# Optimization experiments

Measured on AMD Instinct MI355X. Metric: run time of the kernel, lower is better.

## Reference

```python
import jax, jax.numpy as jnp
import numpy as np

B, C, H, W = 1024, 3, 32, 32
NCLS = 10

def _conv(x, w, b, padding):
    y = jax.lax.conv_general_dilated(x, w, (1, 1), padding, dimension_numbers=('NCHW', 'OIHW', 'NCHW'))
    return y + b[None, :, None, None]

def _maxpool2(x):
    return jax.lax.reduce_window(x, -jnp.inf, jax.lax.max, (1, 1, 2, 2), (1, 1, 2, 2), 'VALID')

def _lenet(x, lw1, lb1, lw2, lb2, lfc1, lfb1, lfc2, lfb2, lfc3, lfb3):
    h = jax.nn.relu(_conv(x, lw1, lb1, 'VALID'))   # [B,6,28,28]
    h = _maxpool2(h)                               # [B,6,14,14]
    h = jax.nn.relu(_conv(h, lw2, lb2, 'VALID'))   # [B,16,10,10]
    h = _maxpool2(h)                               # [B,16,5,5]
    h = h.reshape(h.shape[0], -1)                  # [B,400]
    h = jax.nn.relu(h @ lfc1 + lfb1)
    h = jax.nn.relu(h @ lfc2 + lfb2)
    return h @ lfc3 + lfb3                         # [B,10]

def _resnet(x, rw0, rb0, rw1a, rb1a, rw1b, rb1b, rw2a, rb2a, rw2b, rb2b, rfc, rfb):
    h = jax.nn.relu(_conv(x, rw0, rb0, 'SAME'))    # [B,64,32,32]
    r = jax.nn.relu(_conv(h, rw1a, rb1a, 'SAME'))
    r = _conv(r, rw1b, rb1b, 'SAME')
    h = jax.nn.relu(h + r)
    r = jax.nn.relu(_conv(h, rw2a, rb2a, 'SAME'))
    r = _conv(r, rw2b, rb2b, 'SAME')
    h = jax.nn.relu(h + r)
    h = h.mean(axis=(2, 3))                        # [B,64]
    return h @ rfc + rfb                           # [B,10]

def setup_inputs():
    key = jax.random.key(0)
    ks = jax.random.split(key, 16)
    def w(k, shape, fan_in):
        return jax.random.normal(k, shape, jnp.float32) * np.float32(1.0 / np.sqrt(fan_in))
    return {
        'x': jax.random.normal(ks[0], (B, C, H, W), jnp.float32),
        'threshold': jnp.float32(0.3),
        'labels': jax.random.randint(ks[1], (B,), 0, NCLS),
        'lw1': w(ks[2], (6, 3, 5, 5), 75), 'lb1': jnp.zeros((6,), jnp.float32),
        'lw2': w(ks[3], (16, 6, 5, 5), 150), 'lb2': jnp.zeros((16,), jnp.float32),
        'lfc1': w(ks[4], (400, 120), 400), 'lfb1': jnp.zeros((120,), jnp.float32),
        'lfc2': w(ks[5], (120, 84), 120), 'lfb2': jnp.zeros((84,), jnp.float32),
        'lfc3': w(ks[6], (84, NCLS), 84), 'lfb3': jnp.zeros((NCLS,), jnp.float32),
        'rw0': w(ks[7], (64, 3, 3, 3), 27), 'rb0': jnp.zeros((64,), jnp.float32),
        'rw1a': w(ks[8], (64, 64, 3, 3), 576), 'rb1a': jnp.zeros((64,), jnp.float32),
        'rw1b': w(ks[9], (64, 64, 3, 3), 576), 'rb1b': jnp.zeros((64,), jnp.float32),
        'rw2a': w(ks[10], (64, 64, 3, 3), 576), 'rb2a': jnp.zeros((64,), jnp.float32),
        'rw2b': w(ks[11], (64, 64, 3, 3), 576), 'rb2b': jnp.zeros((64,), jnp.float32),
        'rfc': w(ks[12], (64, NCLS), 64), 'rfb': jnp.zeros((NCLS,), jnp.float32),
    }

def reference(x, threshold, labels, lw1, lb1, lw2, lb2, lfc1, lfb1, lfc2, lfb2, lfc3, lfb3, rw0, rb0, rw1a, rb1a, rw1b, rb1b, rw2a, rb2a, rw2b, rb2b, rfc, rfb):
    out = _lenet(x, lw1, lb1, lw2, lb2, lfc1, lfb1, lfc2, lfb2, lfc3, lfb3)
    pred = jnp.argmax(out, axis=1)
    # fused confusion-matrix update: single scatter-add replaces the 10x10 python loop
    conf_matrix = jnp.zeros((NCLS, NCLS), jnp.float32).at[labels, pred].add(1.0)
    probs = jax.nn.softmax(out, axis=1)
    top2, _ = jax.lax.top_k(probs, 2)
    low_conf = (top2[:, 0] - top2[:, 1]) <= threshold    # [B] bool
    # batched fallback: one grouped resnet call + masked merge replaces the per-sample loop
    res_out = _resnet(x, rw0, rb0, rw1a, rb1a, rw1b, rb1b, rw2a, rb2a, rw2b, rb2b, rfc, rfb)
    out = jnp.where(low_conf[:, None], res_out, out)
    return out, conf_matrix
```

## Files before the change

### kernel.cpp

```cpp
#include <hip/hip_runtime.h>
#include <hip/hip_bf16.h>
#include <math.h>

#define BATCH 1024

typedef __attribute__((ext_vector_type(8))) short bf16x8;
typedef __attribute__((ext_vector_type(4))) float f32x4;

#define IMG_ELEMS 73984
#define IMG_B 147968
#define ROW_B 4352
#define CH_B 544
#define WT_OFF 43520
#define WT_HALF_B 36864
#define BOUNCE_OFF 25088
#define STAGE_A_U 1568

__global__ __launch_bounds__(256) void lenet_conv1(const float* __restrict__ x,
    const float* __restrict__ w, const float* __restrict__ bias, float* __restrict__ p1)
{
    __shared__ float img[3 * 1024];
    __shared__ float wl[450];
    __shared__ float bl[6];
    int b = blockIdx.x, t = threadIdx.x;
    for (int i = t; i < 3072; i += 256) img[i] = x[(size_t)b * 3072 + i];
    for (int i = t; i < 450; i += 256) wl[i] = w[i];
    if (t < 6) bl[t] = bias[t];
    __syncthreads();
    for (int idx = t; idx < 1176; idx += 256) {
        int o = idx / 196, r = idx - o * 196, py = r / 14, px = r - py * 14;
        int y0 = 2 * py, x0 = 2 * px;
        float s00, s01, s10, s11;
        s00 = s01 = s10 = s11 = bl[o];
        for (int c = 0; c < 3; c++) {
            float pv[6][6];
            #pragma unroll
            for (int i2 = 0; i2 < 6; i2++)
                #pragma unroll
                for (int j2 = 0; j2 < 6; j2++)
                    pv[i2][j2] = img[c * 1024 + (y0 + i2) * 32 + x0 + j2];
            const float* wc = &wl[o * 75 + c * 25];
            #pragma unroll
            for (int ky = 0; ky < 5; ky++)
                #pragma unroll
                for (int kx = 0; kx < 5; kx++) {
                    float wv = wc[ky * 5 + kx];
                    s00 += pv[ky][kx] * wv;
                    s01 += pv[ky][kx + 1] * wv;
                    s10 += pv[ky + 1][kx] * wv;
                    s11 += pv[ky + 1][kx + 1] * wv;
                }
        }
        float m = fmaxf(fmaxf(s00, s01), fmaxf(s10, s11));
        p1[(size_t)b * 1176 + idx] = fmaxf(m, 0.f);
    }
}

__global__ __launch_bounds__(256) void lenet_conv2(const float* __restrict__ p1,
    const float* __restrict__ w, const float* __restrict__ bias, float* __restrict__ p2)
{
    __shared__ float img[1176];
    __shared__ float wl[2400];
    __shared__ float bl[16];
    int b = blockIdx.x, t = threadIdx.x;
    for (int i = t; i < 1176; i += 256) img[i] = p1[(size_t)b * 1176 + i];
    for (int i = t; i < 2400; i += 256) wl[i] = w[i];
    if (t < 16) bl[t] = bias[t];
    __syncthreads();
    for (int idx = t; idx < 400; idx += 256) {
        int o = idx / 25, r = idx - o * 25, py = r / 5, px = r - py * 5;
        int y0 = 2 * py, x0 = 2 * px;
        float s00, s01, s10, s11;
        s00 = s01 = s10 = s11 = bl[o];
        for (int c = 0; c < 6; c++) {
            float pv[6][6];
            #pragma unroll
            for (int i2 = 0; i2 < 6; i2++)
                #pragma unroll
                for (int j2 = 0; j2 < 6; j2++)
                    pv[i2][j2] = img[c * 196 + (y0 + i2) * 14 + x0 + j2];
            const float* wc = &wl[o * 150 + c * 25];
            #pragma unroll
            for (int ky = 0; ky < 5; ky++)
                #pragma unroll
                for (int kx = 0; kx < 5; kx++) {
                    float wv = wc[ky * 5 + kx];
                    s00 += pv[ky][kx] * wv;
                    s01 += pv[ky][kx + 1] * wv;
                    s10 += pv[ky + 1][kx] * wv;
                    s11 += pv[ky + 1][kx + 1] * wv;
                }
        }
        float m = fmaxf(fmaxf(s00, s01), fmaxf(s10, s11));
        p2[(size_t)b * 400 + idx] = fmaxf(m, 0.f);
    }
}

__global__ __launch_bounds__(256) void lenet_fc(const float* __restrict__ p2,
    const float* __restrict__ w1, const float* __restrict__ b1,
    const float* __restrict__ w2, const float* __restrict__ b2,
    const float* __restrict__ w3, const float* __restrict__ b3,
    const int* __restrict__ labels, const float* __restrict__ thr,
    float* __restrict__ out, float* __restrict__ conf, int* __restrict__ flags)
{
    __shared__ float xin[400];
    __shared__ float h1[120];
    __shared__ float h2[84];
    __shared__ float ps[256];
    __shared__ float lg[10];
    int b = blockIdx.x, t = threadIdx.x;
    for (int i = t; i < 400; i += 256) xin[i] = p2[(size_t)b * 400 + i];
    __syncthreads();
    {
        int n = t & 127, half = t >> 7;
        float s = 0.f;
        if (n < 120) {
            int k0 = half * 200;
            for (int k = k0; k < k0 + 200; k++) s += xin[k] * w1[k * 120 + n];
        }
        ps[t] = s;
    }
    __syncthreads();
    if (t < 120) h1[t] = fmaxf(ps[t] + ps[t + 128] + b1[t], 0.f);
    __syncthreads();
    {
        int n = t & 127, half = t >> 7;
        float s = 0.f;
        if (n < 84) {
            int k0 = half * 60;
            for (int k = k0; k < k0 + 60; k++) s += h1[k] * w2[k * 84 + n];
        }
        ps[t] = s;
    }
    __syncthreads();
    if (t < 84) h2[t] = fmaxf(ps[t] + ps[t + 128] + b2[t], 0.f);
    __syncthreads();
    if (t < 10) {
        float s = b3[t];
        for (int k = 0; k < 84; k++) s += h2[k] * w3[k * 10 + t];
        lg[t] = s;
        out[(size_t)b * 10 + t] = s;
    }
    __syncthreads();
    if (t == 0) {
        int pred = 0;
        float m = lg[0];
        #pragma unroll
        for (int j = 1; j < 10; j++) if (lg[j] > m) { m = lg[j]; pred = j; }
        float se = 0.f, m2 = -1e30f;
        #pragma unroll
        for (int j = 0; j < 10; j++) {
            se += expf(lg[j] - m);
            if (j != pred) m2 = fmaxf(m2, lg[j]);
        }
        float gap = (1.f - expf(m2 - m)) / se;
        flags[b] = (gap <= thr[0]) ? 1 : 0;
        atomicAdd(&conf[labels[b] * 10 + pred], 1.f);
    }
}

__global__ __launch_bounds__(256) void prep_weights(
    const float* __restrict__ w0, const float* __restrict__ w1,
    const float* __restrict__ w2, const float* __restrict__ w3,
    __hip_bfloat16* __restrict__ dst)
{
    int tid = blockIdx.x * 256 + threadIdx.x;
    if (tid >= 4 * 36864) return;
    int c = tid / 36864, r = tid - c * 36864;
    int tap = r / 4096, r2 = r - tap * 4096;
    int co = r2 >> 6, ci = r2 & 63;
    const float* src = (c == 0) ? w0 : (c == 1) ? w1 : (c == 2) ? w2 : w3;
    float v = src[((size_t)co * 64 + ci) * 9 + tap];
    int nh = co >> 5, nt = (co >> 4) & 1, m = co & 15;
    int kb = ci >> 5, q = (ci >> 3) & 3, e = ci & 7;
    size_t elem = (size_t)(c * 2 + nh) * 18432
                + (size_t)((tap * 2 + kb) * 2 + nt) * 512 + q * 128 + m * 8 + e;
    dst[elem] = __float2bfloat16(v);
}

__global__ __launch_bounds__(256) void prep_w0t(const float* __restrict__ w,
                                                float* __restrict__ dst)
{
    int tid = blockIdx.x * 256 + threadIdx.x;
    if (tid >= 1728) return;
    int k = tid >> 6, co = tid & 63;
    dst[tid] = w[co * 27 + k];
}

__global__ __launch_bounds__(256) void zero_borders(__hip_bfloat16* __restrict__ buf, int cb)
{
    int tid = blockIdx.x * 256 + threadIdx.x;
    int total = cb * 132 * 8;
    if (tid >= total) return;
    int img = tid / 1056, r = tid - img * 1056;
    int pxi = r >> 3, chunk = r & 7;
    int row, col;
    if (pxi < 34)       { row = 0;  col = pxi; }
    else if (pxi < 68)  { row = 33; col = pxi - 34; }
    else if (pxi < 100) { row = pxi - 67; col = 0; }
    else                { row = pxi - 99; col = 33; }
    uint4 z = {0, 0, 0, 0};
    *(uint4*)((char*)buf + (size_t)img * IMG_B + (size_t)row * ROW_B
              + chunk * CH_B + col * 16) = z;
}

__global__ __launch_bounds__(256) void conv0_nhwc(const float* __restrict__ x,
    const float* __restrict__ wT, const float* __restrict__ bias,
    __hip_bfloat16* __restrict__ out, int cb)
{
    __shared__ char smem[8 * ROW_B];
    float* sl = (float*)smem;
    int bid = blockIdx.x;
    int img = bid % cb, strip = bid / cb;
    int r0 = strip * 8;
    int t = threadIdx.x;
    const float* xi = x + (size_t)img * 3072;
    for (int i = t; i < 1020; i += 256) {
        int c = i / 340, rr2 = i - c * 340;
        int rr = rr2 / 34, cc = rr2 - rr * 34;
        int y = r0 + rr - 1, xx = cc - 1;
        float v = 0.f;
        if (y >= 0 && y < 32 && xx >= 0 && xx < 32) v = xi[c * 1024 + y * 32 + xx];
        sl[(c * 10 + rr) * 34 + cc] = v;
    }
    __syncthreads();

    int rr = t >> 5, col = t & 31;
    float iv[27];
    #pragma unroll
    for (int c = 0; c < 3; c++)
        #pragma unroll
        for (int dy = 0; dy < 3; dy++)
            #pragma unroll
            for (int dx = 0; dx < 3; dx++)
                iv[c * 9 + dy * 3 + dx] = sl[(c * 10 + rr + dy) * 34 + col + dx];
    __syncthreads();

    float s[64];
    #pragma unroll
    for (int co = 0; co < 64; co++) s[co] = bias[co];
    #pragma unroll
    for (int k = 0; k < 27; k++) {
        const float v = iv[k];
        const float* wk = wT + k * 64;
        #pragma unroll
        for (int co = 0; co < 64; co++) s[co] = fmaf(v, wk[co], s[co]);
    }
    __hip_bfloat16 ov[64];
    #pragma unroll
    for (int co = 0; co < 64; co++) ov[co] = __float2bfloat16(fmaxf(s[co], 0.f));

    char* brow = smem + rr * ROW_B + (col + 1) * 16;
    const uint4* srcv = (const uint4*)ov;
    #pragma unroll
    for (int j = 0; j < 8; j++) *(uint4*)(brow + j * CH_B) = srcv[j];
    if (t < 128) {
        int row = t >> 4, ch = (t >> 1) & 7, side = t & 1;
        uint4 z = {0, 0, 0, 0};
        *(uint4*)(smem + row * ROW_B + ch * CH_B + (side ? 33 : 0) * 16) = z;
    }
    __syncthreads();
    char* gbase = (char*)out + (size_t)img * IMG_B + (size_t)(r0 + 1) * ROW_B;
    for (int u = t; u < 2176; u += 256)
        *(uint4*)(gbase + (size_t)u * 16) = *(const uint4*)(smem + (size_t)u * 16);
}

#define GLL(gp, lp)                                                            \
    __builtin_amdgcn_global_load_lds(                                          \
        (const __attribute__((address_space(1))) unsigned int*)(gp),           \
        (__attribute__((address_space(3))) unsigned int*)(lp), 16, 0, 0)

template<bool ADD>
__global__ __launch_bounds__(256, 2) void conv3x3_lds(
    const __hip_bfloat16* __restrict__ act, const __hip_bfloat16* __restrict__ wts,
    const float* __restrict__ bias, const __hip_bfloat16* __restrict__ skip,
    __hip_bfloat16* __restrict__ out, int cb)
{
    __shared__ char sl[WT_OFF + WT_HALF_B];
    int bid = blockIdx.x;
    int img = bid % cb, nh = bid / cb;
    int t = threadIdx.x;
    int w = t >> 6, lane = t & 63;
    int m = lane & 15, q = lane >> 4;

    const char* gimg = (const char*)act + (size_t)img * IMG_B;

    const char* gw = (const char*)wts + (size_t)nh * WT_HALF_B;
    for (int u0 = w * 64; u0 < 2304; u0 += 256)
        GLL(gw + (size_t)(u0 + lane) * 16, sl + WT_OFF + u0 * 16);
    for (int u0 = w * 64; u0 < 2720; u0 += 256) {
        int u = u0 + lane;
        if (u < 2720) GLL(gimg + (size_t)u * 16, sl + u0 * 16);
    }
    asm volatile("s_waitcnt vmcnt(0)" ::: "memory");
    __builtin_amdgcn_s_barrier();

    int abase[4];
    #pragma unroll
    for (int mt = 0; mt < 4; mt++)
        abase[mt] = (2 * w + (mt >> 1)) * ROW_B + ((mt & 1) * 16 + m) * 16 + q * CH_B;
    int bbase[2];
    #pragma unroll
    for (int nt = 0; nt < 2; nt++)
        bbase[nt] = WT_OFF + nt * 1024 + q * 256 + m * 16;
    float bv[2] = { bias[nh * 32 + m], bias[nh * 32 + 16 + m] };

    for (int strip = 0; strip < 4; ++strip) {
        f32x4 acc[4][2] = {};
        bf16x8 a[2][4], b[2][2];

        #define ALOAD(s, buf)                                                  \
            {                                                                  \
                const int tap_ = (s) >> 1, kb_ = (s) & 1;                      \
                const int dy_ = tap_ / 3, dx_ = tap_ - dy_ * 3;                \
                const int aoff_ = dy_ * ROW_B + kb_ * (4 * CH_B) + dx_ * 16;   \
                _Pragma("unroll")                                              \
                for (int mt = 0; mt < 4; mt++)                                 \
                    a[buf][mt] = *(const bf16x8*)(sl + abase[mt] + aoff_);     \
            }
        #define BLOAD(s, buf)                                                  \
            {                                                                  \
                const int boff_ = ((s) >> 1) * 4096 + ((s) & 1) * 2048;        \
                _Pragma("unroll")                                              \
                for (int nt = 0; nt < 2; nt++)                                 \
                    b[buf][nt] = *(const bf16x8*)(sl + bbase[nt] + boff_);     \
            }

        ALOAD(0, 0) BLOAD(0, 0)
        #pragma unroll
        for (int s = 0; s < 18; s++) {
            int cur = s & 1;
            if (s < 17) { ALOAD(s + 1, cur ^ 1) BLOAD(s + 1, cur ^ 1) }
            #pragma unroll
            for (int mt = 0; mt < 4; mt++)
                #pragma unroll
                for (int nt = 0; nt < 2; nt++)
                    acc[mt][nt] = __builtin_amdgcn_mfma_f32_16x16x32_bf16(
                        a[cur][mt], b[cur][nt], acc[mt][nt], 0, 0, 0);
        }
        #undef ALOAD
        #undef BLOAD

        asm volatile("s_waitcnt lgkmcnt(0)" ::: "memory");
        __builtin_amdgcn_s_barrier();
        const char* gn = gimg + (size_t)(strip + 1) * (8 * ROW_B);
        if (strip < 3)
            for (int u0 = w * 64; u0 < STAGE_A_U; u0 += 256) {
                int u = u0 + lane;
                if (u < STAGE_A_U) GLL(gn + (size_t)u * 16, sl + u0 * 16);
            }

        #pragma unroll
        for (int nt = 0; nt < 2; nt++) {
            #pragma unroll
            for (int mt = 0; mt < 4; mt++) {
                int pl = (2 * w + (mt >> 1)) * 32 + (mt & 1) * 16 + q * 4;
                #pragma unroll
                for (int r = 0; r < 4; r++) {
                    __hip_bfloat16 hv = __float2bfloat16(acc[mt][nt][r] + bv[nt]);
                    *(__hip_bfloat16*)(sl + BOUNCE_OFF + (size_t)(pl + r) * 72
                                       + (nt * 16 + m) * 2) = hv;
                }
            }
        }
        asm volatile("s_waitcnt lgkmcnt(0)" ::: "memory");
        __builtin_amdgcn_s_barrier();

        {
            char* oimg = (char*)out + (size_t)img * IMG_B;
            const char* simg = (const char*)skip + (size_t)img * IMG_B;
            int ch = (t >> 5) & 3, px = t & 31, rhalf = t >> 7;
            #pragma unroll
            for (int pass = 0; pass < 4; pass++) {
                int rl = pass * 2 + rhalf;
                size_t goff = (size_t)(strip * 8 + 1 + rl) * ROW_B
                            + (nh * 4 + ch) * CH_B + (px + 1) * 16;
                bf16x8 v = *(const bf16x8*)(sl + BOUNCE_OFF
                            + (size_t)(rl * 32 + px) * 72 + ch * 16);
                bf16x8 o;
                if (ADD) {
                    bf16x8 sv = *(const bf16x8*)(simg + goff);
                    #pragma unroll
                    for (int e = 0; e < 8; e++) {
                        float f = __bfloat162float(((__hip_bfloat16*)&v)[e])
                                + __bfloat162float(((__hip_bfloat16*)&sv)[e]);
                        ((__hip_bfloat16*)&o)[e] = __float2bfloat16(fmaxf(f, 0.f));
                    }
                } else {
                    #pragma unroll
                    for (int e = 0; e < 8; e++) {
                        float f = __bfloat162float(((__hip_bfloat16*)&v)[e]);
                        ((__hip_bfloat16*)&o)[e] = __float2bfloat16(fmaxf(f, 0.f));
                    }
                }
                *(bf16x8*)(oimg + goff) = o;
            }
        }

        if (strip < 3) {
            asm volatile("s_waitcnt lgkmcnt(0)" ::: "memory");
            __builtin_amdgcn_s_barrier();
            for (int u0 = STAGE_A_U + w * 64; u0 < 2720; u0 += 256) {
                int u = u0 + lane;
                if (u < 2720) GLL(gn + (size_t)u * 16, sl + u0 * 16);
            }
            asm volatile("s_waitcnt vmcnt(0)" ::: "memory");
            __builtin_amdgcn_s_barrier();
        }
    }
}

__global__ __launch_bounds__(256) void res_head_bf16(const __hip_bfloat16* __restrict__ h,
    const float* __restrict__ rfc, const float* __restrict__ rfb,
    const int* __restrict__ flags, float* __restrict__ out)
{
    __shared__ float part[4][64];
    __shared__ float mns[64];
    int img = blockIdx.x, t = threadIdx.x;
    int w = t >> 6, lane = t & 63;
    int c = lane & 7;
    const char* base = (const char*)h + (size_t)img * IMG_B;

    float s8[8];
    #pragma unroll
    for (int j = 0; j < 8; j++) s8[j] = 0.f;

    for (int ry = 0; ry < 8; ry++) {
        int row = w * 8 + ry + 1;
        const char* rb = base + (size_t)row * ROW_B;
        #pragma unroll
        for (int k = 0; k < 4; k++) {
            int g = lane + 64 * k;
            bf16x8 v = *(const bf16x8*)(rb + c * CH_B + ((g >> 3) + 1) * 16);
            #pragma unroll
            for (int j = 0; j < 8; j++)
                s8[j] += __bfloat162float(*(__hip_bfloat16*)&((short*)&v)[j]);
        }
    }
    #pragma unroll
    for (int off = 8; off <= 32; off <<= 1)
        #pragma unroll
        for (int j = 0; j < 8; j++) s8[j] += __shfl_xor(s8[j], off, 64);
    if (lane < 8)
        #pragma unroll
        for (int j = 0; j < 8; j++) part[w][c * 8 + j] = s8[j];
    __syncthreads();
    if (t < 64) mns[t] = (part[0][t] + part[1][t] + part[2][t] + part[3][t]) * (1.f / 1024.f);
    __syncthreads();
    if (t < 10 && flags[img]) {
        float s2 = rfb[t];
        for (int cc = 0; cc < 64; cc++) s2 += mns[cc] * rfc[cc * 10 + t];
        out[(size_t)img * 10 + t] = s2;
    }
}

extern "C" void kernel_launch(void* const* d_in, const int* in_sizes, int n_in,
                              void* d_out, int out_size, void* d_ws, size_t ws_size,
                              hipStream_t stream)
{
    const float* x    = (const float*)d_in[0];
    const float* thr  = (const float*)d_in[1];
    const int*   labels = (const int*)d_in[2];
    const float* lw1 = (const float*)d_in[3];  const float* lb1 = (const float*)d_in[4];
    const float* lw2 = (const float*)d_in[5];  const float* lb2 = (const float*)d_in[6];
    const float* lfc1 = (const float*)d_in[7]; const float* lfb1 = (const float*)d_in[8];
    const float* lfc2 = (const float*)d_in[9]; const float* lfb2 = (const float*)d_in[10];
    const float* lfc3 = (const float*)d_in[11];const float* lfb3 = (const float*)d_in[12];
    const float* rw0 = (const float*)d_in[13]; const float* rb0 = (const float*)d_in[14];
    const float* rw1a = (const float*)d_in[15];const float* rb1a = (const float*)d_in[16];
    const float* rw1b = (const float*)d_in[17];const float* rb1b = (const float*)d_in[18];
    const float* rw2a = (const float*)d_in[19];const float* rb2a = (const float*)d_in[20];
    const float* rw2b = (const float*)d_in[21];const float* rb2b = (const float*)d_in[22];
    const float* rfc = (const float*)d_in[23]; const float* rfb = (const float*)d_in[24];

    float* out  = (float*)d_out;
    float* conf = out + (size_t)BATCH * 10;

    int nc = 1;
    while (nc < 16 &&
           2ull * (size_t)(BATCH / nc) * 147968ull + 294912ull + 16384ull > ws_size)
        nc <<= 1;
    int cb = BATCH / nc;

    __hip_bfloat16* A  = (__hip_bfloat16*)d_ws;
    __hip_bfloat16* Bb = A + (size_t)cb * IMG_ELEMS;
    __hip_bfloat16* wprep = Bb + (size_t)cb * IMG_ELEMS;
    int* flags = (int*)((char*)wprep + 294912);
    float* w0t = (float*)((char*)wprep + 294912 + 4096);

    float* p1 = (float*)A;
    float* p2 = p1 + 1204224;

    hipMemsetAsync(conf, 0, 100 * sizeof(float), stream);

    prep_weights<<<(4 * 36864 + 255) / 256, 256, 0, stream>>>(rw1a, rw1b, rw2a, rw2b, wprep);
    prep_w0t<<<7, 256, 0, stream>>>(rw0, w0t);

    lenet_conv1<<<BATCH, 256, 0, stream>>>(x, lw1, lb1, p1);
    lenet_conv2<<<BATCH, 256, 0, stream>>>(p1, lw2, lb2, p2);
    lenet_fc<<<BATCH, 256, 0, stream>>>(p2, lfc1, lfb1, lfc2, lfb2, lfc3, lfb3,
                                        labels, thr, out, conf, flags);

    int zb = (cb * 1056 + 255) / 256;
    zero_borders<<<zb, 256, 0, stream>>>(A, cb);
    zero_borders<<<zb, 256, 0, stream>>>(Bb, cb);

    const __hip_bfloat16* W1a = wprep;
    const __hip_bfloat16* W1b = wprep + 36864;
    const __hip_bfloat16* W2a = wprep + 2 * 36864;
    const __hip_bfloat16* W2b = wprep + 3 * 36864;

    for (int c0 = 0; c0 < BATCH; c0 += cb) {
        const float* xc = x + (size_t)c0 * 3072;
        conv0_nhwc<<<cb * 4, 256, 0, stream>>>(xc, w0t, rb0, A, cb);
        conv3x3_lds<false><<<cb * 2, 256, 0, stream>>>(A,  W1a, rb1a, nullptr, Bb, cb);
        conv3x3_lds<true ><<<cb * 2, 256, 0, stream>>>(Bb, W1b, rb1b, A, A, cb);
        conv3x3_lds<false><<<cb * 2, 256, 0, stream>>>(A,  W2a, rb2a, nullptr, Bb, cb);
        conv3x3_lds<true ><<<cb * 2, 256, 0, stream>>>(Bb, W2b, rb2b, A, A, cb);
        res_head_bf16<<<cb, 256, 0, stream>>>(A, rfc, rfb, flags + c0, out + (size_t)c0 * 10);
    }
}
```

Before: 713.5 us.

## Compute all 64 output channels per block in conv3x3 and drop split staging

```diff
diff --git a/kernel.cpp b/kernel.cpp
--- a/kernel.cpp
+++ b/kernel.cpp
@@ -13,8 +13,6 @@
 #define CH_B 544
 #define WT_OFF 43520
 #define WT_HALF_B 36864
-#define BOUNCE_OFF 25088
-#define STAGE_A_U 1568
 
 __global__ __launch_bounds__(256) void lenet_conv1(const float* __restrict__ x,
     const float* __restrict__ w, const float* __restrict__ bias, float* __restrict__ p1)
@@ -271,43 +269,43 @@
         (__attribute__((address_space(3))) unsigned int*)(lp), 16, 0, 0)
 
 template<bool ADD>
-__global__ __launch_bounds__(256, 2) void conv3x3_lds(
+__global__ __launch_bounds__(256, 1) void conv3x3_lds(
     const __hip_bfloat16* __restrict__ act, const __hip_bfloat16* __restrict__ wts,
     const float* __restrict__ bias, const __hip_bfloat16* __restrict__ skip,
     __hip_bfloat16* __restrict__ out, int cb)
 {
-    __shared__ char sl[WT_OFF + WT_HALF_B];
-    int bid = blockIdx.x;
-    int img = bid % cb, nh = bid / cb;
+    __shared__ char sl[WT_OFF + 2 * WT_HALF_B];
+    int img = blockIdx.x;
     int t = threadIdx.x;
     int w = t >> 6, lane = t & 63;
     int m = lane & 15, q = lane >> 4;
 
     const char* gimg = (const char*)act + (size_t)img * IMG_B;
 
-    const char* gw = (const char*)wts + (size_t)nh * WT_HALF_B;
-    for (int u0 = w * 64; u0 < 2304; u0 += 256)
+    const char* gw = (const char*)wts;
+    for (int u0 = w * 64; u0 < 4608; u0 += 256)
         GLL(gw + (size_t)(u0 + lane) * 16, sl + WT_OFF + u0 * 16);
     for (int u0 = w * 64; u0 < 2720; u0 += 256) {
         int u = u0 + lane;
         if (u < 2720) GLL(gimg + (size_t)u * 16, sl + u0 * 16);
     }
-    asm volatile("s_waitcnt vmcnt(0)" ::: "memory");
-    __builtin_amdgcn_s_barrier();
+    __syncthreads();
 
     int abase[4];
     #pragma unroll
     for (int mt = 0; mt < 4; mt++)
         abase[mt] = (2 * w + (mt >> 1)) * ROW_B + ((mt & 1) * 16 + m) * 16 + q * CH_B;
-    int bbase[2];
-    #pragma unroll
-    for (int nt = 0; nt < 2; nt++)
-        bbase[nt] = WT_OFF + nt * 1024 + q * 256 + m * 16;
-    float bv[2] = { bias[nh * 32 + m], bias[nh * 32 + 16 + m] };
+    int bbase[4];
+    #pragma unroll
+    for (int nt = 0; nt < 4; nt++)
+        bbase[nt] = WT_OFF + (nt >> 1) * WT_HALF_B + (nt & 1) * 1024 + q * 256 + m * 16;
+    float bv[4];
+    #pragma unroll
+    for (int nt = 0; nt < 4; nt++) bv[nt] = bias[nt * 16 + m];
 
     for (int strip = 0; strip < 4; ++strip) {
-        f32x4 acc[4][2] = {};
-        bf16x8 a[2][4], b[2][2];
+        f32x4 acc[4][4] = {};
+        bf16x8 a[2][4], b[2][4];
 
         #define ALOAD(s, buf)                                                  \
             {                                                                  \
@@ -322,7 +320,7 @@
             {                                                                  \
                 const int boff_ = ((s) >> 1) * 4096 + ((s) & 1) * 2048;        \
                 _Pragma("unroll")                                              \
-                for (int nt = 0; nt < 2; nt++)                                 \
+                for (int nt = 0; nt < 4; nt++)                                 \
                     b[buf][nt] = *(const bf16x8*)(sl + bbase[nt] + boff_);     \
             }
 
@@ -334,49 +332,39 @@
             #pragma unroll
             for (int mt = 0; mt < 4; mt++)
                 #pragma unroll
-                for (int nt = 0; nt < 2; nt++)
+                for (int nt = 0; nt < 4; nt++)
                     acc[mt][nt] = __builtin_amdgcn_mfma_f32_16x16x32_bf16(
                         a[cur][mt], b[cur][nt], acc[mt][nt], 0, 0, 0);
         }
         #undef ALOAD
         #undef BLOAD
 
-        asm volatile("s_waitcnt lgkmcnt(0)" ::: "memory");
-        __builtin_amdgcn_s_barrier();
-        const char* gn = gimg + (size_t)(strip + 1) * (8 * ROW_B);
-        if (strip < 3)
-            for (int u0 = w * 64; u0 < STAGE_A_U; u0 += 256) {
-                int u = u0 + lane;
-                if (u < STAGE_A_U) GLL(gn + (size_t)u * 16, sl + u0 * 16);
-            }
-
-        #pragma unroll
-        for (int nt = 0; nt < 2; nt++) {
+        __syncthreads();
+
+        #pragma unroll
+        for (int nt = 0; nt < 4; nt++) {
             #pragma unroll
             for (int mt = 0; mt < 4; mt++) {
                 int pl = (2 * w + (mt >> 1)) * 32 + (mt & 1) * 16 + q * 4;
                 #pragma unroll
                 for (int r = 0; r < 4; r++) {
                     __hip_bfloat16 hv = __float2bfloat16(acc[mt][nt][r] + bv[nt]);
-                    *(__hip_bfloat16*)(sl + BOUNCE_OFF + (size_t)(pl + r) * 72
+                    *(__hip_bfloat16*)(sl + (size_t)(pl + r) * 136
                                        + (nt * 16 + m) * 2) = hv;
                 }
             }
         }
-        asm volatile("s_waitcnt lgkmcnt(0)" ::: "memory");
-        __builtin_amdgcn_s_barrier();
+        __syncthreads();
 
         {
             char* oimg = (char*)out + (size_t)img * IMG_B;
             const char* simg = (const char*)skip + (size_t)img * IMG_B;
-            int ch = (t >> 5) & 3, px = t & 31, rhalf = t >> 7;
-            #pragma unroll
-            for (int pass = 0; pass < 4; pass++) {
-                int rl = pass * 2 + rhalf;
-                size_t goff = (size_t)(strip * 8 + 1 + rl) * ROW_B
-                            + (nh * 4 + ch) * CH_B + (px + 1) * 16;
-                bf16x8 v = *(const bf16x8*)(sl + BOUNCE_OFF
-                            + (size_t)(rl * 32 + px) * 72 + ch * 16);
+            int ch = t >> 5, px = t & 31;
+            #pragma unroll
+            for (int pass = 0; pass < 8; pass++) {
+                size_t goff = (size_t)(strip * 8 + 1 + pass) * ROW_B
+                            + ch * CH_B + (px + 1) * 16;
+                bf16x8 v = *(const bf16x8*)(sl + (size_t)(pass * 32 + px) * 136 + ch * 16);
                 bf16x8 o;
                 if (ADD) {
                     bf16x8 sv = *(const bf16x8*)(simg + goff);
@@ -398,14 +386,13 @@
         }
 
         if (strip < 3) {
-            asm volatile("s_waitcnt lgkmcnt(0)" ::: "memory");
-            __builtin_amdgcn_s_barrier();
-            for (int u0 = STAGE_A_U + w * 64; u0 < 2720; u0 += 256) {
+            __syncthreads();
+            const char* gn = gimg + (size_t)(strip + 1) * (8 * ROW_B);
+            for (int u0 = w * 64; u0 < 2720; u0 += 256) {
                 int u = u0 + lane;
                 if (u < 2720) GLL(gn + (size_t)u * 16, sl + u0 * 16);
             }
-            asm volatile("s_waitcnt vmcnt(0)" ::: "memory");
-            __builtin_amdgcn_s_barrier();
+            __syncthreads();
         }
     }
 }
@@ -513,10 +500,10 @@
     for (int c0 = 0; c0 < BATCH; c0 += cb) {
         const float* xc = x + (size_t)c0 * 3072;
         conv0_nhwc<<<cb * 4, 256, 0, stream>>>(xc, w0t, rb0, A, cb);
-        conv3x3_lds<false><<<cb * 2, 256, 0, stream>>>(A,  W1a, rb1a, nullptr, Bb, cb);
-        conv3x3_lds<true ><<<cb * 2, 256, 0, stream>>>(Bb, W1b, rb1b, A, A, cb);
-        conv3x3_lds<false><<<cb * 2, 256, 0, stream>>>(A,  W2a, rb2a, nullptr, Bb, cb);
-        conv3x3_lds<true ><<<cb * 2, 256, 0, stream>>>(Bb, W2b, rb2b, A, A, cb);
+        conv3x3_lds<false><<<cb, 256, 0, stream>>>(A,  W1a, rb1a, nullptr, Bb, cb);
+        conv3x3_lds<true ><<<cb, 256, 0, stream>>>(Bb, W1b, rb1b, A, A, cb);
+        conv3x3_lds<false><<<cb, 256, 0, stream>>>(A,  W2a, rb2a, nullptr, Bb, cb);
+        conv3x3_lds<true ><<<cb, 256, 0, stream>>>(Bb, W2b, rb2b, A, A, cb);
         res_head_bf16<<<cb, 256, 0, stream>>>(A, rfc, rfb, flags + c0, out + (size_t)c0 * 10);
     }
 }
```

New measurement: 726.2 us. Within noise of the previous version (+1.8%).
